# Optimization experiments

Measured on AMD Instinct MI355X. Metric: run time of the kernel, lower is better.

Reference implementation:

```python
import jax, jax.numpy as jnp
import numpy as np

N, C_IN, T, V = 8, 256, 128, 128
OUT, H = 512, 8
D = OUT // H  # head_dim = 64
SCALE = D ** (-0.5)  # original code DIVIDES score by this (multiplies by sqrt(D))


def setup_inputs() -> dict:
    key = jax.random.key(0)
    ks = jax.random.split(key, 6)
    x = jax.random.normal(ks[0], (N, C_IN, T, V), dtype=jnp.float32)
    wq = jax.random.normal(ks[1], (OUT, C_IN), dtype=jnp.float32) * (C_IN ** -0.5)
    wk = jax.random.normal(ks[2], (OUT, C_IN), dtype=jnp.float32) * (C_IN ** -0.5)
    wv = jax.random.normal(ks[3], (OUT, C_IN), dtype=jnp.float32) * (C_IN ** -0.5)
    wp = jax.random.normal(ks[4], (OUT, OUT), dtype=jnp.float32) * (OUT ** -0.5)
    bp = jnp.zeros((OUT,), dtype=jnp.float32)
    return {"x": x, "wq": wq, "wk": wk, "wv": wv, "wp": wp, "bp": bp}


def _split_heads(y):
    # (N, OUT, T, V) -> (N, T, H, V, D)
    n, _, t, v = y.shape
    return jnp.transpose(y.reshape(n, H, D, t, v), (0, 3, 1, 4, 2))


def reference(x, wq, wk, wv, wp, bp):
    # 1x1 conv projections == channel matmul
    q = _split_heads(jnp.einsum('oc,nctv->notv', wq, x))
    k = _split_heads(jnp.einsum('oc,nctv->notv', wk, x))
    v = _split_heads(jnp.einsum('oc,nctv->notv', wv, x))
    # attention over joint axis V; NOTE: faithful reproduction of original
    # which divides by scale = D**-0.5 (i.e. multiplies by sqrt(D))
    score = jnp.einsum('nthvd,nthwd->nthvw', q, k) / SCALE
    attn = jax.nn.softmax(score, axis=-1)
    o = jnp.einsum('nthvw,nthwd->nthvd', attn, v)  # (N,T,H,V,D)
    # transpose(3,4) -> (N,T,H,D,V); reshape -> (N,T,OUT,V); transpose(1,2) -> (N,OUT,T,V)
    o = jnp.transpose(o, (0, 1, 2, 4, 3)).reshape(o.shape[0], o.shape[1], OUT, o.shape[3])
    o = jnp.swapaxes(o, 1, 2)
    out = jnp.einsum('oc,nctv->notv', wp, o) + bp[None, :, None, None]
    return out
```

## Files before the change

kernel.cpp:

```cpp
#include <hip/hip_runtime.h>
#include <hip/hip_bf16.h>
#include <stddef.h>

#define NN    8
#define CIN   256
#define TT    128
#define VV    128
#define OUTC  512
#define HH    8
#define DD    64

typedef _Float16 f16;
typedef _Float16 f16x8 __attribute__((ext_vector_type(8)));
typedef float    f32x4 __attribute__((ext_vector_type(4)));

#define MFMA16(a, b, c) __builtin_amdgcn_mfma_f32_16x16x32_f16((a), (b), (c), 0, 0, 0)

#define XE_OFF   ((size_t)0)
#define WQ_OFF   ((size_t)67108864)
#define WK_OFF   ((size_t)67371008)
#define WV_OFF   ((size_t)67633152)
#define WP_OFF   ((size_t)67895296)
#define OE_OFF   ((size_t)68419584)

__device__ __forceinline__ size_t fragoff(int o, int c, int nc)
{
    return (size_t)(o >> 4) * (nc * 16) + ((c >> 5) << 9) + (((c >> 3) & 3) << 7)
         + ((o & 15) << 3) + (c & 7);
}

__global__ __launch_bounds__(256, 4)
void prep_kernel(const float* __restrict__ x,
                 const float* __restrict__ wq,
                 const float* __restrict__ wk,
                 const float* __restrict__ wv,
                 const float* __restrict__ wp,
                 f16* __restrict__ xe,
                 f16* __restrict__ wq16, f16* __restrict__ wk16,
                 f16* __restrict__ wv16, f16* __restrict__ wp16)
{
    const int bid = blockIdx.x;
    const int tid = threadIdx.x;

    if (bid < NN * TT) {
        __shared__ f16 tile[128 * 136];
        const int n = bid >> 7;
        const int t = bid & 127;

        for (int p = 0; p < 2; ++p) {
            #pragma unroll
            for (int it = 0; it < 4; ++it) {
                const int cl = it * 32 + (tid >> 3);
                const int c  = p * 128 + cl;
                const int v0 = (tid & 7) * 16;
                const float* src = x + (((size_t)(n * CIN + c) * TT + t) * VV) + v0;
                #pragma unroll
                for (int q = 0; q < 4; ++q) {
                    const float4 xv = *(const float4*)(src + q * 4);
                    union { uint2 u; f16 h[4]; } pk;
                    pk.h[0] = (f16)xv.x; pk.h[1] = (f16)xv.y;
                    pk.h[2] = (f16)xv.z; pk.h[3] = (f16)xv.w;
                    *(uint2*)&tile[cl * 136 + v0 + q * 4] = pk.u;
                }
            }
            __syncthreads();
            {
                const int v  = tid >> 1;
                const int ch = tid & 1;
                f16* dstbase = xe + (size_t)(n * TT + t) * VV * 256;
                #pragma unroll
                for (int q8 = 0; q8 < 8; ++q8) {
                    const int c0 = p * 128 + ch * 64 + q8 * 8;
                    union { int4 u; f16 h[8]; } pk;
                    #pragma unroll
                    for (int s = 0; s < 8; ++s)
                        pk.h[s] = tile[(ch * 64 + q8 * 8 + s) * 136 + v];
                    *(int4*)(dstbase + fragoff(v, c0, 256)) = pk.u;
                }
            }
            __syncthreads();
        }
    } else {
        const int gid = (bid - NN * TT) * 256 + tid;
        for (int i = gid; i < 163840; i += 4096) {
            const int e = i * 4;
            union { uint2 u; f16 h[4]; } pk;
            if (e < 131072) {
                const float4 v = *(const float4*)(wq + e);
                pk.h[0] = (f16)(v.x * 8.0f); pk.h[1] = (f16)(v.y * 8.0f);
                pk.h[2] = (f16)(v.z * 8.0f); pk.h[3] = (f16)(v.w * 8.0f);
                *(uint2*)(wq16 + fragoff(e >> 8, e & 255, 256)) = pk.u;
            } else if (e < 262144) {
                const int e2 = e - 131072;
                const float4 v = *(const float4*)(wk + e2);
                pk.h[0] = (f16)v.x; pk.h[1] = (f16)v.y; pk.h[2] = (f16)v.z; pk.h[3] = (f16)v.w;
                *(uint2*)(wk16 + fragoff(e2 >> 8, e2 & 255, 256)) = pk.u;
            } else if (e < 393216) {
                const int e2 = e - 262144;
                const float4 v = *(const float4*)(wv + e2);
                pk.h[0] = (f16)v.x; pk.h[1] = (f16)v.y; pk.h[2] = (f16)v.z; pk.h[3] = (f16)v.w;
                *(uint2*)(wv16 + fragoff(e2 >> 8, e2 & 255, 256)) = pk.u;
            } else {
                const int e2 = e - 393216;
                const float4 v = *(const float4*)(wp + e2);
                pk.h[0] = (f16)v.x; pk.h[1] = (f16)v.y; pk.h[2] = (f16)v.z; pk.h[3] = (f16)v.w;
                *(uint2*)(wp16 + fragoff(e2 >> 9, e2 & 511, 512)) = pk.u;
            }
        }
    }
}

__device__ __forceinline__ f16x8 regroup32(f32x4 T0, f32x4 T1, int g, int r)
{
    union { unsigned u; f16 h[2]; } pa, pb, pc, pd;
    pa.h[0] = (f16)T0[0]; pa.h[1] = (f16)T0[1];
    pb.h[0] = (f16)T0[2]; pb.h[1] = (f16)T0[3];
    pc.h[0] = (f16)T1[0]; pc.h[1] = (f16)T1[1];
    pd.h[0] = (f16)T1[2]; pd.h[1] = (f16)T1[3];
    const int s0 = r + ((g & 1) << 5);
    const int s1 = s0 + 16;
    const bool lo = (g < 2);
    const unsigned a0 = (unsigned)__shfl((int)pa.u, s0, 64);
    const unsigned c0 = (unsigned)__shfl((int)pc.u, s0, 64);
    const unsigned b0 = (unsigned)__shfl((int)pb.u, s0, 64);
    const unsigned d0 = (unsigned)__shfl((int)pd.u, s0, 64);
    const unsigned a1 = (unsigned)__shfl((int)pa.u, s1, 64);
    const unsigned c1 = (unsigned)__shfl((int)pc.u, s1, 64);
    const unsigned b1 = (unsigned)__shfl((int)pb.u, s1, 64);
    const unsigned d1 = (unsigned)__shfl((int)pd.u, s1, 64);
    union { unsigned u[4]; f16x8 v; } out;
    out.u[0] = lo ? a0 : c0;
    out.u[1] = lo ? b0 : d0;
    out.u[2] = lo ? a1 : c1;
    out.u[3] = lo ? b1 : d1;
    return out.v;
}

__global__ __launch_bounds__(256, 4)
void qkv_attn_kernel(const f16* __restrict__ xe,
                     const f16* __restrict__ wq16,
                     const f16* __restrict__ wk16,
                     const f16* __restrict__ wv16,
                     f16* __restrict__ oe)
{
    __shared__ f16 smem[17920];
    f16* sK  = smem;
    f16* sVT = smem + 9216;

    const int tid = threadIdx.x;
    const int wid = tid >> 6;
    const int l   = tid & 63;
    const int r   = l & 15;
    const int g   = l >> 4;

    const int i   = blockIdx.x;
    const int xcd = i & 7;
    const int m   = i >> 3;
    const int nt  = xcd * 128 + (m >> 3);
    const int h   = m & 7;
    const int n   = nt >> 7;
    const int t   = nt & 127;

    const f16* xrow = xe + (size_t)(n * TT + t) * VV * 256;

    f32x4 accq[4][2], acck[4][2];
    #pragma unroll
    for (int dt = 0; dt < 4; ++dt)
        #pragma unroll
        for (int vt = 0; vt < 2; ++vt) { accq[dt][vt] = (f32x4)0.0f; acck[dt][vt] = (f32x4)0.0f; }

    for (int ks = 0; ks < 8; ++ks) {
        f16x8 aq[4], ak[4], bx[2];
        #pragma unroll
        for (int dt = 0; dt < 4; ++dt) {
            aq[dt] = *(const f16x8*)(wq16 + (size_t)(h * 4 + dt) * 4096 + ks * 512 + l * 8);
            ak[dt] = *(const f16x8*)(wk16 + (size_t)(h * 4 + dt) * 4096 + ks * 512 + l * 8);
        }
        #pragma unroll
        for (int vt = 0; vt < 2; ++vt)
            bx[vt] = *(const f16x8*)(xrow + (size_t)(wid * 2 + vt) * 4096 + ks * 512 + l * 8);
        #pragma unroll
        for (int dt = 0; dt < 4; ++dt)
            #pragma unroll
            for (int vt = 0; vt < 2; ++vt) {
                accq[dt][vt] = MFMA16(aq[dt], bx[vt], accq[dt][vt]);
                acck[dt][vt] = MFMA16(ak[dt], bx[vt], acck[dt][vt]);
            }
    }
    #pragma unroll
    for (int dt = 0; dt < 4; ++dt)
        #pragma unroll
        for (int vt = 0; vt < 2; ++vt) {
            const int v = wid * 32 + vt * 16 + r;
            union { uint2 u; f16 h4[4]; } pk;
            #pragma unroll
            for (int i2 = 0; i2 < 4; ++i2)
                pk.h4[i2] = (f16)acck[dt][vt][i2];
            *(uint2*)&sK[v * 72 + dt * 16 + g * 4] = pk.u;
        }
    f16x8 qfrag[2][2];
    #pragma unroll
    for (int vt = 0; vt < 2; ++vt) {
        qfrag[vt][0] = regroup32(accq[0][vt], accq[1][vt], g, r);
        qfrag[vt][1] = regroup32(accq[2][vt], accq[3][vt], g, r);
    }

    f32x4 accv[4][2];
    #pragma unroll
    for (int dt = 0; dt < 4; ++dt)
        #pragma unroll
        for (int wt = 0; wt < 2; ++wt) accv[dt][wt] = (f32x4)0.0f;

    for (int ks = 0; ks < 8; ++ks) {
        f16x8 av[4], bx[2];
        #pragma unroll
        for (int dt = 0; dt < 4; ++dt)
            av[dt] = *(const f16x8*)(wv16 + (size_t)(h * 4 + dt) * 4096 + ks * 512 + l * 8);
        #pragma unroll
        for (int wt = 0; wt < 2; ++wt)
            bx[wt] = *(const f16x8*)(xrow + (size_t)(wid * 2 + wt) * 4096 + ks * 512 + l * 8);
        #pragma unroll
        for (int dt = 0; dt < 4; ++dt)
            #pragma unroll
            for (int wt = 0; wt < 2; ++wt)
                accv[dt][wt] = MFMA16(av[dt], bx[wt], accv[dt][wt]);
    }
    #pragma unroll
    for (int dt = 0; dt < 4; ++dt)
        #pragma unroll
        for (int wt = 0; wt < 2; ++wt) {
            const int w = wid * 32 + wt * 16 + r;
            #pragma unroll
            for (int i2 = 0; i2 < 4; ++i2)
                sVT[(dt * 16 + g * 4 + i2) * 136 + w] = (f16)accv[dt][wt][i2];
        }
    __syncthreads();

    f32x4 sT[8][2];
    #pragma unroll
    for (int mt = 0; mt < 8; ++mt)
        #pragma unroll
        for (int vt = 0; vt < 2; ++vt) sT[mt][vt] = (f32x4)0.0f;

    #pragma unroll
    for (int ks = 0; ks < 2; ++ks) {
        const int ko = ks * 32 + g * 8;
        #pragma unroll
        for (int mt = 0; mt < 8; ++mt) {
            const f16x8 a = *(const f16x8*)&sK[(mt * 16 + r) * 72 + ko];
            #pragma unroll
            for (int vt = 0; vt < 2; ++vt)
                sT[mt][vt] = MFMA16(a, qfrag[vt][ks], sT[mt][vt]);
        }
    }

    float inv[2];
    #pragma unroll
    for (int vt = 0; vt < 2; ++vt) {
        float mx = -3.0e38f;
        #pragma unroll
        for (int mt = 0; mt < 8; ++mt)
            #pragma unroll
            for (int i2 = 0; i2 < 4; ++i2) mx = fmaxf(mx, sT[mt][vt][i2]);
        mx = fmaxf(mx, __shfl_xor(mx, 16));
        mx = fmaxf(mx, __shfl_xor(mx, 32));
        float sm = 0.0f;
        #pragma unroll
        for (int mt = 0; mt < 8; ++mt)
            #pragma unroll
            for (int i2 = 0; i2 < 4; ++i2) {
                const float e = __expf(sT[mt][vt][i2] - mx);
                sT[mt][vt][i2] = e;
                sm += e;
            }
        sm += __shfl_xor(sm, 16);
        sm += __shfl_xor(sm, 32);
        inv[vt] = 1.0f / sm;
    }

    f32x4 oT[4][2];
    #pragma unroll
    for (int dt = 0; dt < 4; ++dt)
        #pragma unroll
        for (int vt = 0; vt < 2; ++vt) oT[dt][vt] = (f32x4)0.0f;

    #pragma unroll
    for (int ks = 0; ks < 4; ++ks) {
        const int ko = ks * 32 + g * 8;
        f16x8 pf[2];
        #pragma unroll
        for (int vt = 0; vt < 2; ++vt)
            pf[vt] = regroup32(sT[2 * ks][vt], sT[2 * ks + 1][vt], g, r);
        #pragma unroll
        for (int dt = 0; dt < 4; ++dt) {
            const f16x8 a = *(const f16x8*)&sVT[(dt * 16 + r) * 136 + ko];
            #pragma unroll
            for (int vt = 0; vt < 2; ++vt)
                oT[dt][vt] = MFMA16(a, pf[vt], oT[dt][vt]);
        }
    }

    f16* oerow = oe + (size_t)(n * TT + t) * VV * 512;
    #pragma unroll
    for (int dt = 0; dt < 4; ++dt)
        #pragma unroll
        for (int vt = 0; vt < 2; ++vt) {
            union { uint2 u; f16 h4[4]; } pk;
            #pragma unroll
            for (int i2 = 0; i2 < 4; ++i2) pk.h4[i2] = (f16)(oT[dt][vt][i2] * inv[vt]);
            f16* dst = oerow + (size_t)(wid * 2 + vt) * 8192
                     + (h * 2 + (dt >> 1)) * 512
                     + ((dt & 1) * 2 + (g >> 1)) * 128
                     + r * 8 + (g & 1) * 4;
            *(uint2*)dst = pk.u;
        }
}

__global__ __launch_bounds__(256, 4)
void out_proj_kernel(const f16* __restrict__ oe,
                     const f16* __restrict__ wp16,
                     const float* __restrict__ bp,
                     float* __restrict__ out)
{
    const int tid = threadIdx.x;
    const int wid = tid >> 6;
    const int l   = tid & 63;
    const int r   = l & 15;
    const int g   = l >> 4;

    const int i   = blockIdx.x;
    const int xcd = i & 7;
    const int m   = i >> 3;
    const int nt  = xcd * 128 + (m >> 2);
    const int sub = m & 3;
    const int og  = sub >> 1;
    const int vh  = sub & 1;
    const int n   = nt >> 7;
    const int t   = nt & 127;

    const f16* brow = oe + (size_t)(n * TT + t) * VV * 512;

    f32x4 acc[4][4];
    #pragma unroll
    for (int mi = 0; mi < 4; ++mi)
        #pragma unroll
        for (int nt2 = 0; nt2 < 4; ++nt2) acc[mi][nt2] = (f32x4)0.0f;

    for (int ks = 0; ks < 16; ++ks) {
        f16x8 a[4], b[4];
        #pragma unroll
        for (int mi = 0; mi < 4; ++mi)
            a[mi] = *(const f16x8*)(wp16 + (size_t)(og * 16 + wid * 4 + mi) * 8192 + ks * 512 + l * 8);
        #pragma unroll
        for (int nt2 = 0; nt2 < 4; ++nt2)
            b[nt2] = *(const f16x8*)(brow + (size_t)(vh * 4 + nt2) * 8192 + ks * 512 + l * 8);
        #pragma unroll
        for (int mi = 0; mi < 4; ++mi)
            #pragma unroll
            for (int nt2 = 0; nt2 < 4; ++nt2)
                acc[mi][nt2] = MFMA16(a[mi], b[nt2], acc[mi][nt2]);
    }

    #pragma unroll
    for (int mi = 0; mi < 4; ++mi) {
        const int obase = og * 256 + (wid * 4 + mi) * 16 + g * 4;
        const float b0 = bp[obase + 0];
        const float b1 = bp[obase + 1];
        const float b2 = bp[obase + 2];
        const float b3 = bp[obase + 3];
        #pragma unroll
        for (int nt2 = 0; nt2 < 4; ++nt2) {
            const int v = vh * 64 + nt2 * 16 + r;
            float* dst = out + ((size_t)(n * OUTC + obase) * TT + t) * VV + v;
            dst[0 * TT * VV] = acc[mi][nt2][0] + b0;
            dst[1 * TT * VV] = acc[mi][nt2][1] + b1;
            dst[2 * TT * VV] = acc[mi][nt2][2] + b2;
            dst[3 * TT * VV] = acc[mi][nt2][3] + b3;
        }
    }
}

extern "C" void kernel_launch(void* const* d_in, const int* in_sizes, int n_in,
                              void* d_out, int out_size, void* d_ws, size_t ws_size,
                              hipStream_t stream)
{
    const float* x  = (const float*)d_in[0];
    const float* wq = (const float*)d_in[1];
    const float* wk = (const float*)d_in[2];
    const float* wv = (const float*)d_in[3];
    const float* wp = (const float*)d_in[4];
    const float* bp = (const float*)d_in[5];
    float* out = (float*)d_out;

    char* ws = (char*)d_ws;
    f16* xe   = (f16*)(ws + XE_OFF);
    f16* wq16 = (f16*)(ws + WQ_OFF);
    f16* wk16 = (f16*)(ws + WK_OFF);
    f16* wv16 = (f16*)(ws + WV_OFF);
    f16* wp16 = (f16*)(ws + WP_OFF);
    f16* oe   = (f16*)(ws + OE_OFF);

    prep_kernel<<<NN * TT + 16, 256, 0, stream>>>(x, wq, wk, wv, wp, xe, wq16, wk16, wv16, wp16);
    qkv_attn_kernel<<<NN * TT * HH, 256, 0, stream>>>(xe, wq16, wk16, wv16, oe);
    out_proj_kernel<<<NN * TT * 4, 256, 0, stream>>>(oe, wp16, bp, out);
}
```

Measured before the change: 698.4 us.

## Fuse QKV projection loops, add MFMA priority hints, widen out-proj tile

Merges the separate V projection loop into the Q/K loop, so the x fragments are loaded once per k-step and shared by all three projections. Wraps the MFMA blocks in s_setprio hints so matrix instructions get issue priority. The output projection now covers all 128 joints per block instead of half, halving the grid and reusing the weight fragments across twice as many columns. The trade-off is higher register pressure (extra accumulators, launch bounds lowered to 2 blocks per SM) and lower occupancy.

```diff
diff --git a/kernel.cpp b/kernel.cpp
--- a/kernel.cpp
+++ b/kernel.cpp
@@ -163,30 +163,39 @@
 
     const f16* xrow = xe + (size_t)(n * TT + t) * VV * 256;
 
-    f32x4 accq[4][2], acck[4][2];
-    #pragma unroll
-    for (int dt = 0; dt < 4; ++dt)
-        #pragma unroll
-        for (int vt = 0; vt < 2; ++vt) { accq[dt][vt] = (f32x4)0.0f; acck[dt][vt] = (f32x4)0.0f; }
+    f32x4 accq[4][2], acck[4][2], accv[4][2];
+    #pragma unroll
+    for (int dt = 0; dt < 4; ++dt)
+        #pragma unroll
+        for (int vt = 0; vt < 2; ++vt) {
+            accq[dt][vt] = (f32x4)0.0f;
+            acck[dt][vt] = (f32x4)0.0f;
+            accv[dt][vt] = (f32x4)0.0f;
+        }
 
     for (int ks = 0; ks < 8; ++ks) {
-        f16x8 aq[4], ak[4], bx[2];
+        f16x8 aq[4], ak[4], av[4], bx[2];
         #pragma unroll
         for (int dt = 0; dt < 4; ++dt) {
             aq[dt] = *(const f16x8*)(wq16 + (size_t)(h * 4 + dt) * 4096 + ks * 512 + l * 8);
             ak[dt] = *(const f16x8*)(wk16 + (size_t)(h * 4 + dt) * 4096 + ks * 512 + l * 8);
+            av[dt] = *(const f16x8*)(wv16 + (size_t)(h * 4 + dt) * 4096 + ks * 512 + l * 8);
         }
         #pragma unroll
         for (int vt = 0; vt < 2; ++vt)
             bx[vt] = *(const f16x8*)(xrow + (size_t)(wid * 2 + vt) * 4096 + ks * 512 + l * 8);
+        __builtin_amdgcn_s_setprio(1);
         #pragma unroll
         for (int dt = 0; dt < 4; ++dt)
             #pragma unroll
             for (int vt = 0; vt < 2; ++vt) {
                 accq[dt][vt] = MFMA16(aq[dt], bx[vt], accq[dt][vt]);
                 acck[dt][vt] = MFMA16(ak[dt], bx[vt], acck[dt][vt]);
-            }
-    }
+                accv[dt][vt] = MFMA16(av[dt], bx[vt], accv[dt][vt]);
+            }
+        __builtin_amdgcn_s_setprio(0);
+    }
+
     #pragma unroll
     for (int dt = 0; dt < 4; ++dt)
         #pragma unroll
@@ -198,42 +207,21 @@
                 pk.h4[i2] = (f16)acck[dt][vt][i2];
             *(uint2*)&sK[v * 72 + dt * 16 + g * 4] = pk.u;
         }
+    #pragma unroll
+    for (int dt = 0; dt < 4; ++dt)
+        #pragma unroll
+        for (int wt = 0; wt < 2; ++wt) {
+            const int w = wid * 32 + wt * 16 + r;
+            #pragma unroll
+            for (int i2 = 0; i2 < 4; ++i2)
+                sVT[(dt * 16 + g * 4 + i2) * 136 + w] = (f16)accv[dt][wt][i2];
+        }
     f16x8 qfrag[2][2];
     #pragma unroll
     for (int vt = 0; vt < 2; ++vt) {
         qfrag[vt][0] = regroup32(accq[0][vt], accq[1][vt], g, r);
         qfrag[vt][1] = regroup32(accq[2][vt], accq[3][vt], g, r);
     }
-
-    f32x4 accv[4][2];
-    #pragma unroll
-    for (int dt = 0; dt < 4; ++dt)
-        #pragma unroll
-        for (int wt = 0; wt < 2; ++wt) accv[dt][wt] = (f32x4)0.0f;
-
-    for (int ks = 0; ks < 8; ++ks) {
-        f16x8 av[4], bx[2];
-        #pragma unroll
-        for (int dt = 0; dt < 4; ++dt)
-            av[dt] = *(const f16x8*)(wv16 + (size_t)(h * 4 + dt) * 4096 + ks * 512 + l * 8);
-        #pragma unroll
-        for (int wt = 0; wt < 2; ++wt)
-            bx[wt] = *(const f16x8*)(xrow + (size_t)(wid * 2 + wt) * 4096 + ks * 512 + l * 8);
-        #pragma unroll
-        for (int dt = 0; dt < 4; ++dt)
-            #pragma unroll
-            for (int wt = 0; wt < 2; ++wt)
-                accv[dt][wt] = MFMA16(av[dt], bx[wt], accv[dt][wt]);
-    }
-    #pragma unroll
-    for (int dt = 0; dt < 4; ++dt)
-        #pragma unroll
-        for (int wt = 0; wt < 2; ++wt) {
-            const int w = wid * 32 + wt * 16 + r;
-            #pragma unroll
-            for (int i2 = 0; i2 < 4; ++i2)
-                sVT[(dt * 16 + g * 4 + i2) * 136 + w] = (f16)accv[dt][wt][i2];
-        }
     __syncthreads();
 
     f32x4 sT[8][2];
@@ -248,9 +236,11 @@
         #pragma unroll
         for (int mt = 0; mt < 8; ++mt) {
             const f16x8 a = *(const f16x8*)&sK[(mt * 16 + r) * 72 + ko];
+            __builtin_amdgcn_s_setprio(1);
             #pragma unroll
             for (int vt = 0; vt < 2; ++vt)
                 sT[mt][vt] = MFMA16(a, qfrag[vt][ks], sT[mt][vt]);
+            __builtin_amdgcn_s_setprio(0);
         }
     }
 
@@ -294,9 +284,11 @@
         #pragma unroll
         for (int dt = 0; dt < 4; ++dt) {
             const f16x8 a = *(const f16x8*)&sVT[(dt * 16 + r) * 136 + ko];
+            __builtin_amdgcn_s_setprio(1);
             #pragma unroll
             for (int vt = 0; vt < 2; ++vt)
                 oT[dt][vt] = MFMA16(a, pf[vt], oT[dt][vt]);
+            __builtin_amdgcn_s_setprio(0);
         }
     }
 
@@ -316,7 +308,7 @@
         }
 }
 
-__global__ __launch_bounds__(256, 4)
+__global__ __launch_bounds__(256, 2)
 void out_proj_kernel(const f16* __restrict__ oe,
                      const f16* __restrict__ wp16,
                      const float* __restrict__ bp,
@@ -331,34 +323,34 @@
     const int i   = blockIdx.x;
     const int xcd = i & 7;
     const int m   = i >> 3;
-    const int nt  = xcd * 128 + (m >> 2);
-    const int sub = m & 3;
-    const int og  = sub >> 1;
-    const int vh  = sub & 1;
+    const int nt  = xcd * 128 + (m >> 1);
+    const int og  = m & 1;
     const int n   = nt >> 7;
     const int t   = nt & 127;
 
     const f16* brow = oe + (size_t)(n * TT + t) * VV * 512;
 
-    f32x4 acc[4][4];
+    f32x4 acc[4][8];
     #pragma unroll
     for (int mi = 0; mi < 4; ++mi)
         #pragma unroll
-        for (int nt2 = 0; nt2 < 4; ++nt2) acc[mi][nt2] = (f32x4)0.0f;
+        for (int nt2 = 0; nt2 < 8; ++nt2) acc[mi][nt2] = (f32x4)0.0f;
 
     for (int ks = 0; ks < 16; ++ks) {
-        f16x8 a[4], b[4];
+        f16x8 a[4], b[8];
         #pragma unroll
         for (int mi = 0; mi < 4; ++mi)
             a[mi] = *(const f16x8*)(wp16 + (size_t)(og * 16 + wid * 4 + mi) * 8192 + ks * 512 + l * 8);
         #pragma unroll
-        for (int nt2 = 0; nt2 < 4; ++nt2)
-            b[nt2] = *(const f16x8*)(brow + (size_t)(vh * 4 + nt2) * 8192 + ks * 512 + l * 8);
+        for (int nt2 = 0; nt2 < 8; ++nt2)
+            b[nt2] = *(const f16x8*)(brow + (size_t)nt2 * 8192 + ks * 512 + l * 8);
+        __builtin_amdgcn_s_setprio(1);
         #pragma unroll
         for (int mi = 0; mi < 4; ++mi)
             #pragma unroll
-            for (int nt2 = 0; nt2 < 4; ++nt2)
+            for (int nt2 = 0; nt2 < 8; ++nt2)
                 acc[mi][nt2] = MFMA16(a[mi], b[nt2], acc[mi][nt2]);
+        __builtin_amdgcn_s_setprio(0);
     }
 
     #pragma unroll
@@ -369,8 +361,8 @@
         const float b2 = bp[obase + 2];
         const float b3 = bp[obase + 3];
         #pragma unroll
-        for (int nt2 = 0; nt2 < 4; ++nt2) {
-            const int v = vh * 64 + nt2 * 16 + r;
+        for (int nt2 = 0; nt2 < 8; ++nt2) {
+            const int v = nt2 * 16 + r;
             float* dst = out + ((size_t)(n * OUTC + obase) * TT + t) * VV + v;
             dst[0 * TT * VV] = acc[mi][nt2][0] + b0;
             dst[1 * TT * VV] = acc[mi][nt2][1] + b1;
@@ -402,5 +394,5 @@
 
     prep_kernel<<<NN * TT + 16, 256, 0, stream>>>(x, wq, wk, wv, wp, xe, wq16, wk16, wv16, wp16);
     qkv_attn_kernel<<<NN * TT * HH, 256, 0, stream>>>(xe, wq16, wk16, wv16, oe);
-    out_proj_kernel<<<NN * TT * 4, 256, 0, stream>>>(oe, wp16, bp, out);
-}
+    out_proj_kernel<<<NN * TT * 2, 256, 0, stream>>>(oe, wp16, bp, out);
+}
```

Result: slower. 1.288 ms (+84.5%).

## Drop LDS transpose in prep and widen out-proj tiles with vectorized stores

Applied to the files above, without the earlier changes.

The prep kernel now loads float2 pairs across 8 channels per thread and packs them straight into the fragment layout, removing the shared-memory tile and its two barriers. The output projection swaps the MFMA operand order so each lane holds 4 consecutive v values, which allows float4 stores along v instead of scalar stores strided by channel. Each block also covers all 128 v (8 n-tiles), halving the grid so each weight fragment is reused across twice as many columns. The cost is more accumulator registers, so occupancy drops (launch bounds lowered from 4 to 2), and the prep reads become narrower strided float2 loads.

```diff
diff --git a/kernel.cpp b/kernel.cpp
--- a/kernel.cpp
+++ b/kernel.cpp
@@ -43,42 +43,25 @@
     const int tid = threadIdx.x;
 
     if (bid < NN * TT) {
-        __shared__ f16 tile[128 * 136];
         const int n = bid >> 7;
         const int t = bid & 127;
-
-        for (int p = 0; p < 2; ++p) {
-            #pragma unroll
-            for (int it = 0; it < 4; ++it) {
-                const int cl = it * 32 + (tid >> 3);
-                const int c  = p * 128 + cl;
-                const int v0 = (tid & 7) * 16;
-                const float* src = x + (((size_t)(n * CIN + c) * TT + t) * VV) + v0;
-                #pragma unroll
-                for (int q = 0; q < 4; ++q) {
-                    const float4 xv = *(const float4*)(src + q * 4);
-                    union { uint2 u; f16 h[4]; } pk;
-                    pk.h[0] = (f16)xv.x; pk.h[1] = (f16)xv.y;
-                    pk.h[2] = (f16)xv.z; pk.h[3] = (f16)xv.w;
-                    *(uint2*)&tile[cl * 136 + v0 + q * 4] = pk.u;
-                }
+        const int v0   = (tid & 63) * 2;
+        const int csub = tid >> 6;
+        f16* dstbase = xe + (size_t)(n * TT + t) * VV * 256;
+
+        #pragma unroll
+        for (int ct = 0; ct < 8; ++ct) {
+            const int c0 = ct * 32 + csub * 8;
+            union { int4 u[2]; f16 h[16]; } pk;
+            #pragma unroll
+            for (int q = 0; q < 8; ++q) {
+                const float2 xv = *(const float2*)(x + (((size_t)(n * CIN + c0 + q) * TT + t) * VV) + v0);
+                pk.h[q]     = (f16)xv.x;
+                pk.h[8 + q] = (f16)xv.y;
             }
-            __syncthreads();
-            {
-                const int v  = tid >> 1;
-                const int ch = tid & 1;
-                f16* dstbase = xe + (size_t)(n * TT + t) * VV * 256;
-                #pragma unroll
-                for (int q8 = 0; q8 < 8; ++q8) {
-                    const int c0 = p * 128 + ch * 64 + q8 * 8;
-                    union { int4 u; f16 h[8]; } pk;
-                    #pragma unroll
-                    for (int s = 0; s < 8; ++s)
-                        pk.h[s] = tile[(ch * 64 + q8 * 8 + s) * 136 + v];
-                    *(int4*)(dstbase + fragoff(v, c0, 256)) = pk.u;
-                }
-            }
-            __syncthreads();
+            f16* dst = dstbase + fragoff(v0, c0, 256);
+            *(int4*)dst       = pk.u[0];
+            *(int4*)(dst + 8) = pk.u[1];
         }
     } else {
         const int gid = (bid - NN * TT) * 256 + tid;
@@ -316,7 +299,7 @@
         }
 }
 
-__global__ __launch_bounds__(256, 4)
+__global__ __launch_bounds__(256, 2)
 void out_proj_kernel(const f16* __restrict__ oe,
                      const f16* __restrict__ wp16,
                      const float* __restrict__ bp,
@@ -331,51 +314,48 @@
     const int i   = blockIdx.x;
     const int xcd = i & 7;
     const int m   = i >> 3;
-    const int nt  = xcd * 128 + (m >> 2);
-    const int sub = m & 3;
-    const int og  = sub >> 1;
-    const int vh  = sub & 1;
+    const int nt  = xcd * 128 + (m >> 1);
+    const int og  = m & 1;
     const int n   = nt >> 7;
     const int t   = nt & 127;
 
     const f16* brow = oe + (size_t)(n * TT + t) * VV * 512;
 
-    f32x4 acc[4][4];
+    f32x4 acc[4][8];
     #pragma unroll
     for (int mi = 0; mi < 4; ++mi)
         #pragma unroll
-        for (int nt2 = 0; nt2 < 4; ++nt2) acc[mi][nt2] = (f32x4)0.0f;
+        for (int nt2 = 0; nt2 < 8; ++nt2) acc[mi][nt2] = (f32x4)0.0f;
 
     for (int ks = 0; ks < 16; ++ks) {
-        f16x8 a[4], b[4];
+        f16x8 a[4], b[8];
         #pragma unroll
         for (int mi = 0; mi < 4; ++mi)
             a[mi] = *(const f16x8*)(wp16 + (size_t)(og * 16 + wid * 4 + mi) * 8192 + ks * 512 + l * 8);
         #pragma unroll
-        for (int nt2 = 0; nt2 < 4; ++nt2)
-            b[nt2] = *(const f16x8*)(brow + (size_t)(vh * 4 + nt2) * 8192 + ks * 512 + l * 8);
+        for (int nt2 = 0; nt2 < 8; ++nt2)
+            b[nt2] = *(const f16x8*)(brow + (size_t)nt2 * 8192 + ks * 512 + l * 8);
         #pragma unroll
         for (int mi = 0; mi < 4; ++mi)
             #pragma unroll
-            for (int nt2 = 0; nt2 < 4; ++nt2)
-                acc[mi][nt2] = MFMA16(a[mi], b[nt2], acc[mi][nt2]);
+            for (int nt2 = 0; nt2 < 8; ++nt2)
+                acc[mi][nt2] = MFMA16(b[nt2], a[mi], acc[mi][nt2]);
     }
 
     #pragma unroll
     for (int mi = 0; mi < 4; ++mi) {
-        const int obase = og * 256 + (wid * 4 + mi) * 16 + g * 4;
-        const float b0 = bp[obase + 0];
-        const float b1 = bp[obase + 1];
-        const float b2 = bp[obase + 2];
-        const float b3 = bp[obase + 3];
-        #pragma unroll
-        for (int nt2 = 0; nt2 < 4; ++nt2) {
-            const int v = vh * 64 + nt2 * 16 + r;
-            float* dst = out + ((size_t)(n * OUTC + obase) * TT + t) * VV + v;
-            dst[0 * TT * VV] = acc[mi][nt2][0] + b0;
-            dst[1 * TT * VV] = acc[mi][nt2][1] + b1;
-            dst[2 * TT * VV] = acc[mi][nt2][2] + b2;
-            dst[3 * TT * VV] = acc[mi][nt2][3] + b3;
+        const int o = og * 256 + (wid * 4 + mi) * 16 + r;
+        const float bv = bp[o];
+        float* orow = out + ((size_t)(n * OUTC + o) * TT + t) * VV;
+        #pragma unroll
+        for (int nt2 = 0; nt2 < 8; ++nt2) {
+            const int v = nt2 * 16 + g * 4;
+            float4 f;
+            f.x = acc[mi][nt2][0] + bv;
+            f.y = acc[mi][nt2][1] + bv;
+            f.z = acc[mi][nt2][2] + bv;
+            f.w = acc[mi][nt2][3] + bv;
+            *(float4*)(orow + v) = f;
         }
     }
 }
@@ -402,5 +382,5 @@
 
     prep_kernel<<<NN * TT + 16, 256, 0, stream>>>(x, wq, wk, wv, wp, xe, wq16, wk16, wv16, wp16);
     qkv_attn_kernel<<<NN * TT * HH, 256, 0, stream>>>(xe, wq16, wk16, wv16, oe);
-    out_proj_kernel<<<NN * TT * 4, 256, 0, stream>>>(oe, wp16, bp, out);
-}
+    out_proj_kernel<<<NN * TT * 2, 256, 0, stream>>>(oe, wp16, bp, out);
+}
```

Result: faster. 678.1 us (-2.9%).
